# Performance work log

Measured on AMD Instinct MI355X. Metric: run time of the kernel, lower is better.

## Reference

```python
import jax, jax.numpy as jnp
import numpy as np
from jax import lax

EPS = 1e-12


def _l2norm(v):
    return v / (jnp.sqrt(jnp.sum(v * v)) + EPS)


def _spectral_norm(W, u):
    # one torch-style power iteration; u, v are treated as constants
    v = lax.stop_gradient(_l2norm(W.T @ u))
    u2 = lax.stop_gradient(_l2norm(W @ v))
    sigma = u2 @ (W @ v)
    return W / sigma


def _lstm(gates_x, Whh):
    # gates_x: [B, T, 4H] = x @ Wih^T + b_ih + b_hh, precomputed
    B, T, G = gates_x.shape
    H = G // 4
    WhhT = Whh.T  # [H, 4H]

    def step(carry, gx_t):
        h, c = carry
        gates = gx_t + h @ WhhT  # [B, 4H]
        i = jax.nn.sigmoid(gates[:, 0 * H:1 * H])
        f = jax.nn.sigmoid(gates[:, 1 * H:2 * H])
        g = jnp.tanh(gates[:, 2 * H:3 * H])
        o = jax.nn.sigmoid(gates[:, 3 * H:4 * H])
        c = f * c + i * g
        h = o * jnp.tanh(c)
        return (h, c), h

    h0 = jnp.zeros((B, H), gates_x.dtype)
    c0 = jnp.zeros((B, H), gates_x.dtype)
    _, hs = lax.scan(step, (h0, c0), jnp.swapaxes(gates_x, 0, 1))
    return jnp.swapaxes(hs, 0, 1)  # [B, T, H]


def setup_inputs() -> dict:
    key = jax.random.key(0)
    ks = jax.random.split(key, 8)
    B, T, C, H = 512, 512, 32, 128
    Cin = C + 1  # minibatch-std channel
    init = lambda k, shp: 0.02 * jax.random.normal(k, shp, dtype=jnp.float32)
    return {
        "x": jax.random.normal(ks[0], (B, T, C), dtype=jnp.float32),
        "w_ih_orig": init(ks[1], (4 * H, Cin)),
        "u_ih": _l2norm(jax.random.normal(ks[2], (4 * H,), dtype=jnp.float32)),
        "w_hh_orig": init(ks[3], (4 * H, H)),
        "u_hh": _l2norm(jax.random.normal(ks[4], (4 * H,), dtype=jnp.float32)),
        "b_ih": jnp.zeros((4 * H,), jnp.float32),
        "b_hh": jnp.zeros((4 * H,), jnp.float32),
        "attn_w": init(ks[5], (1, H)),
        "attn_b": jnp.zeros((1,), jnp.float32),
        "fc_w_orig": init(ks[6], (1, H)),
        "u_fc": _l2norm(jax.random.normal(ks[7], (1,), dtype=jnp.float32)),
        "fc_b": jnp.zeros((1,), jnp.float32),
    }


def reference(x, w_ih_orig, u_ih, w_hh_orig, u_hh, b_ih, b_hh,
              attn_w, attn_b, fc_w_orig, u_fc, fc_b):
    B = x.shape[0]
    # minibatch std feature (torch std: unbiased, ddof=1)
    std_per_step = jnp.std(x, axis=0, ddof=1, keepdims=True)        # [1,T,C]
    std_scalar = jnp.mean(std_per_step, axis=-1, keepdims=True)     # [1,T,1]
    std_channel = jnp.broadcast_to(std_scalar, (B,) + std_scalar.shape[1:])
    x = jnp.concatenate([x, std_channel], axis=-1)                  # [B,T,C+1]

    Wih = _spectral_norm(w_ih_orig, u_ih)
    Whh = _spectral_norm(w_hh_orig, u_hh)
    gates_x = jnp.einsum("btc,gc->btg", x, Wih) + b_ih + b_hh       # [B,T,4H]
    h = _lstm(gates_x, Whh)                                          # [B,T,H]

    attn_logits = jnp.einsum("bth,oh->bto", h, attn_w) + attn_b     # [B,T,1]
    attn = jax.nn.softmax(attn_logits, axis=1)
    pooled = jnp.sum(attn * h, axis=1)                               # [B,H]

    Wfc = _spectral_norm(fc_w_orig, u_fc)
    score = pooled @ Wfc.T + fc_b                                    # [B,1]
    return score
```

## Files before the change

### kernel.cpp

```cpp
#include <hip/hip_runtime.h>
#include <math.h>

#define TT 512
#define BB 512
#define CC 32
#define CIN 33
#define HH 128
#define EPSF 1e-12f
#define CH 16
#define NCH (TT / CH)
#define RB 2
#define HSP 160
#define GXP 520

typedef _Float16 half8 __attribute__((ext_vector_type(8)));
typedef _Float16 half2v __attribute__((ext_vector_type(2)));
typedef float f32x4 __attribute__((ext_vector_type(4)));

#define MFMA16H(a, b, c) __builtin_amdgcn_mfma_f32_16x16x32_f16(a, b, c, 0, 0, 0)
#define BARRIER() asm volatile("s_waitcnt lgkmcnt(0)\n\ts_barrier" ::: "memory")

__device__ __forceinline__ float fsig(float x) {
    return __builtin_amdgcn_rcpf(1.f + __expf(-x));
}
__device__ __forceinline__ float ftanh(float x) {
    return 1.f - 2.f * __builtin_amdgcn_rcpf(1.f + __expf(2.f * x));
}
__device__ __forceinline__ float wave_sum_dpp(float x) {
    x += __int_as_float(__builtin_amdgcn_update_dpp(0, __float_as_int(x), 0x111, 0xf, 0xf, true));
    x += __int_as_float(__builtin_amdgcn_update_dpp(0, __float_as_int(x), 0x112, 0xf, 0xf, true));
    x += __int_as_float(__builtin_amdgcn_update_dpp(0, __float_as_int(x), 0x114, 0xf, 0xf, true));
    x += __int_as_float(__builtin_amdgcn_update_dpp(0, __float_as_int(x), 0x118, 0xf, 0xf, true));
    x += __int_as_float(__builtin_amdgcn_update_dpp(0, __float_as_int(x), 0x142, 0xa, 0xf, true));
    x += __int_as_float(__builtin_amdgcn_update_dpp(0, __float_as_int(x), 0x143, 0xc, 0xf, true));
    return x;
}
__device__ __forceinline__ float row_sum_dpp(float x) {
    x += __int_as_float(__builtin_amdgcn_update_dpp(0, __float_as_int(x), 0x111, 0xf, 0xf, true));
    x += __int_as_float(__builtin_amdgcn_update_dpp(0, __float_as_int(x), 0x112, 0xf, 0xf, true));
    x += __int_as_float(__builtin_amdgcn_update_dpp(0, __float_as_int(x), 0x114, 0xf, 0xf, true));
    x += __int_as_float(__builtin_amdgcn_update_dpp(0, __float_as_int(x), 0x118, 0xf, 0xf, true));
    return x;
}
__device__ __forceinline__ float load_s(const float* p) {
    float v = __hip_atomic_load(p, __ATOMIC_RELAXED, __HIP_MEMORY_SCOPE_AGENT);
    for (int it = 0; it < 100000000 && __float_as_uint(v) == 0xAAAAAAAAu; ++it)
        v = __hip_atomic_load(p, __ATOMIC_RELAXED, __HIP_MEMORY_SCOPE_AGENT);
    return v;
}

__global__ __attribute__((amdgpu_flat_work_group_size(512, 512), amdgpu_waves_per_eu(2, 2)))
void critic_fused(
    const float* __restrict__ x,
    const float* __restrict__ w_ih, const float* __restrict__ u_ih,
    const float* __restrict__ w_hh, const float* __restrict__ u_hh,
    const float* __restrict__ b_ih, const float* __restrict__ b_hh,
    const float* __restrict__ attn_w, const float* __restrict__ attn_b,
    const float* __restrict__ fc_w, const float* __restrict__ u_fc,
    const float* __restrict__ fc_b,
    float* __restrict__ ws,
    float* __restrict__ out)
{
    const int tid = threadIdx.x;
    const int w   = tid >> 6;
    const int l   = tid & 63;
    const int m   = l & 15;
    const int q   = l >> 4;
    const int r   = q & 1;
    const int b0  = blockIdx.x * RB;
    const int jcol = 16 * w + m;

    __shared__ float4 sSS[2][8][8];
    __shared__ float4 sQQ[2][8][8];
    __shared__ float stdp[2][8];
    __shared__ float red[512];
    __shared__ float vv[128];
    __shared__ float sigS[3];
    __shared__ __align__(16) _Float16 hs[2][RB][HSP];
    __shared__ float gxs[2][2 * CH][GXP];
    __shared__ __align__(8) float bcast[2][RB];
    __shared__ float Sf[RB];
    __shared__ float part[8][RB];

    const int c4 = tid & 7;
    const int bs = tid >> 3;
    float4 xa[2][8];
#pragma unroll
    for (int tt = 0; tt < 2; ++tt) {
        const int t = 2 * blockIdx.x + tt;
#pragma unroll
        for (int i = 0; i < 8; ++i)
            xa[tt][i] = *reinterpret_cast<const float4*>(
                x + ((size_t)(bs * 8 + i) * TT + t) * CC + c4 * 4);
    }

    {
        const int c = tid & 127, qq = tid >> 7;
        const float* wp = w_hh + (size_t)(qq * 128) * HH + c;
        const float* up = u_hh + qq * 128;
        float a0 = 0.f, a1 = 0.f, a2 = 0.f, a3 = 0.f;
#pragma unroll 4
        for (int g = 0; g < 128; g += 4) {
            a0 = fmaf(wp[(size_t)(g + 0) * HH], up[g + 0], a0);
            a1 = fmaf(wp[(size_t)(g + 1) * HH], up[g + 1], a1);
            a2 = fmaf(wp[(size_t)(g + 2) * HH], up[g + 2], a2);
            a3 = fmaf(wp[(size_t)(g + 3) * HH], up[g + 3], a3);
        }
        red[tid] = (a0 + a1) + (a2 + a3);
    }

#pragma unroll
    for (int tt = 0; tt < 2; ++tt) {
        float4 S = make_float4(0.f, 0.f, 0.f, 0.f);
        float4 Q = make_float4(0.f, 0.f, 0.f, 0.f);
#pragma unroll
        for (int i = 0; i < 8; ++i) {
            float4 v = xa[tt][i];
            S.x += v.x; S.y += v.y; S.z += v.z; S.w += v.w;
            Q.x = fmaf(v.x, v.x, Q.x); Q.y = fmaf(v.y, v.y, Q.y);
            Q.z = fmaf(v.z, v.z, Q.z); Q.w = fmaf(v.w, v.w, Q.w);
        }
#pragma unroll
        for (int off = 8; off <= 32; off <<= 1) {
            S.x += __shfl_xor(S.x, off, 64); S.y += __shfl_xor(S.y, off, 64);
            S.z += __shfl_xor(S.z, off, 64); S.w += __shfl_xor(S.w, off, 64);
            Q.x += __shfl_xor(Q.x, off, 64); Q.y += __shfl_xor(Q.y, off, 64);
            Q.z += __shfl_xor(Q.z, off, 64); Q.w += __shfl_xor(Q.w, off, 64);
        }
        if (l < 8) { sSS[tt][w][c4] = S; sQQ[tt][w][c4] = Q; }
    }
    __syncthreads();

    if (tid < 128) vv[tid] = red[tid] + red[tid + 128] + red[tid + 256] + red[tid + 384];
    if (tid >= 384 && tid < 400) {
        const int tt2 = (tid - 384) >> 3, cc = (tid - 384) & 7;
        float4 St = make_float4(0.f, 0.f, 0.f, 0.f);
        float4 Qt = make_float4(0.f, 0.f, 0.f, 0.f);
#pragma unroll
        for (int i = 0; i < 8; ++i) {
            float4 a = sSS[tt2][i][cc], b4 = sQQ[tt2][i][cc];
            St.x += a.x; St.y += a.y; St.z += a.z; St.w += a.w;
            Qt.x += b4.x; Qt.y += b4.y; Qt.z += b4.z; Qt.w += b4.w;
        }
        float st = 0.f;
#pragma unroll
        for (int i = 0; i < 4; ++i) {
            float s1 = (i == 0) ? St.x : (i == 1) ? St.y : (i == 2) ? St.z : St.w;
            float q1 = (i == 0) ? Qt.x : (i == 1) ? Qt.y : (i == 2) ? Qt.z : Qt.w;
            float mean = s1 / 512.0f;
            float var  = (q1 - 512.0f * mean * mean) / 511.0f;
            st += sqrtf(fmaxf(var, 0.f));
        }
        stdp[tt2][cc] = st;
    }
    __syncthreads();
    if (tid >= 408 && tid < 410) {
        const int tt2 = tid - 408;
        float mm = 0.f;
#pragma unroll
        for (int i = 0; i < 8; ++i) mm += stdp[tt2][i];
        __hip_atomic_store(&ws[2 * blockIdx.x + tt2], mm / 32.0f, __ATOMIC_RELAXED,
                           __HIP_MEMORY_SCOPE_AGENT);
    }
    red[tid] = (tid < 128) ? vv[tid] * vv[tid] : 0.f;
    __syncthreads();

    {
        for (int s = 64; s >= 1; s >>= 1) { if (tid < s) red[tid] += red[tid + s]; __syncthreads(); }
        const float nv = sqrtf(red[0]);
        __syncthreads();
        if (tid < 128) vv[tid] = vv[tid] / (nv + EPSF);
        __syncthreads();
        float sq = 0.f;
        float2 vl = *reinterpret_cast<const float2*>(&vv[2 * l]);
#pragma unroll 4
        for (int gi = 0; gi < 64; ++gi) {
            const int g = w * 64 + gi;
            float2 wl = *reinterpret_cast<const float2*>(&w_hh[(size_t)g * HH + 2 * l]);
            float p  = fmaf(wl.x, vl.x, wl.y * vl.y);
            float tot = wave_sum_dpp(p);
            sq = fmaf(tot, tot, sq);
        }
        if (l == 63) red[w] = sq;
        __syncthreads();
        if (tid == 0) {
            float ns2 = 0.f;
            for (int i = 0; i < 8; ++i) ns2 += red[i];
            sigS[1] = ns2 / (sqrtf(ns2) + EPSF);
        }
        __syncthreads();
    }
    {
        if (l < CIN) {
            float a0 = 0.f, a1 = 0.f;
#pragma unroll 4
            for (int gi = 0; gi < 64; gi += 2) {
                const int g = w * 64 + gi;
                a0 = fmaf(w_ih[(size_t)(g + 0) * CIN + l], u_ih[g + 0], a0);
                a1 = fmaf(w_ih[(size_t)(g + 1) * CIN + l], u_ih[g + 1], a1);
            }
            red[w * 64 + l] = a0 + a1;
        }
        __syncthreads();
        if (tid < CIN) {
            float v = 0.f;
#pragma unroll
            for (int i = 0; i < 8; ++i) v += red[i * 64 + tid];
            vv[tid] = v;
        }
        __syncthreads();
        if (tid == 0) {
            float n2 = 0.f;
            for (int i = 0; i < CIN; ++i) n2 += vv[i] * vv[i];
            red[400] = sqrtf(n2);
        }
        __syncthreads();
        const float nv = red[400];
        if (tid < CIN) vv[tid] = vv[tid] / (nv + EPSF);
        __syncthreads();
        float vl = (l < CIN) ? vv[l] : 0.f;
        float sq = 0.f;
#pragma unroll 4
        for (int gi = 0; gi < 64; ++gi) {
            const int g = w * 64 + gi;
            float p = (l < CIN) ? w_ih[(size_t)g * CIN + l] * vl : 0.f;
            float tot = wave_sum_dpp(p);
            sq = fmaf(tot, tot, sq);
        }
        if (l == 63) red[w] = sq;
        __syncthreads();
        if (tid == 0) {
            float ns2 = 0.f;
            for (int i = 0; i < 8; ++i) ns2 += red[i];
            sigS[0] = ns2 / (sqrtf(ns2) + EPSF);
        }
        __syncthreads();
    }
    {
        red[tid] = (tid < 128) ? fc_w[tid] * fc_w[tid] : 0.f;
        __syncthreads();
        for (int s = 64; s >= 1; s >>= 1) { if (tid < s) red[tid] += red[tid + s]; __syncthreads(); }
        if (tid == 0) {
            float nw2 = red[0];
            float u0  = u_fc[0];
            float nv  = fabsf(u0) * sqrtf(nw2);
            float wv  = u0 * nw2 / (nv + EPSF);
            sigS[2]   = wv * wv / (fabsf(wv) + EPSF);
        }
        __syncthreads();
    }
    const float rih = 1.f / sigS[0];
    const float rhh = 1.f / sigS[1];
    const float rfc = 1.f / sigS[2];
    const float attb = attn_b[0];

    half8 Bf[4][5];
    float biasg[4], w32g[4];
#pragma unroll
    for (int p = 0; p < 4; ++p) {
        const int g = 16 * w + 128 * p + m;
#pragma unroll
        for (int kt = 0; kt < 4; ++kt) {
            const float* src = w_hh + (size_t)g * HH + kt * 32 + q * 8;
#pragma unroll
            for (int i = 0; i < 8; ++i) Bf[p][kt][i] = (_Float16)(src[i] * rhh);
        }
        {
            const float* src = w_ih + (size_t)g * CIN + q * 8;
#pragma unroll
            for (int i = 0; i < 8; ++i) Bf[p][4][i] = (_Float16)(src[i] * rih);
        }
        w32g[p]  = w_ih[(size_t)g * CIN + 32] * rih;
        biasg[p] = b_ih[g] + b_hh[g];
    }
    f32x4 zero4 = (f32x4){0.f, 0.f, 0.f, 0.f};
#pragma unroll
    for (int p = 0; p < 4; ++p) {
#pragma unroll
        for (int kt = 0; kt < 5; ++kt) asm volatile("" : "+v"(Bf[p][kt]));
        asm volatile("" : "+v"(biasg[p]), "+v"(w32g[p]));
    }
    asm volatile("" : "+v"(zero4));
    const float fcwj = fc_w[jcol] * rfc;
    const float aw0 = attn_w[2 * l];
    const float aw1 = attn_w[2 * l + 1];

#define STAGE_LOAD(t0_, xr_)                                                   \
    {                                                                          \
        _Pragma("unroll")                                                      \
        for (int mt = 0; mt < 2; ++mt) {                                       \
            const size_t base =                                                \
                ((size_t)(b0 + (m & 1)) * TT + ((t0_) + 8 * mt + (m >> 1))) *  \
                    CC + q * 8;                                                \
            xr_[mt][0] = *reinterpret_cast<const float4*>(x + base);           \
            xr_[mt][1] = *reinterpret_cast<const float4*>(x + base + 4);       \
        }                                                                      \
    }

#define STAGE_COMMIT(t0_, nb_, xr_)                                            \
    {                                                                          \
        _Pragma("unroll")                                                      \
        for (int mt = 0; mt < 2; ++mt) {                                       \
            half8 af = {(_Float16)xr_[mt][0].x, (_Float16)xr_[mt][0].y,        \
                        (_Float16)xr_[mt][0].z, (_Float16)xr_[mt][0].w,        \
                        (_Float16)xr_[mt][1].x, (_Float16)xr_[mt][1].y,        \
                        (_Float16)xr_[mt][1].z, (_Float16)xr_[mt][1].w};       \
            f32x4 s0 = MFMA16H(af, Bf[0][4], zero4);                           \
            f32x4 s1 = MFMA16H(af, Bf[1][4], zero4);                           \
            f32x4 s2 = MFMA16H(af, Bf[2][4], zero4);                           \
            f32x4 s3 = MFMA16H(af, Bf[3][4], zero4);                           \
            const float svl = load_s(&ws[(t0_) + 8 * mt + 2 * q]);             \
            const float svh = load_s(&ws[(t0_) + 8 * mt + 2 * q + 1]);         \
            const int row0 = 16 * mt + 4 * q;                                  \
            _Pragma("unroll")                                                  \
            for (int j = 0; j < 4; ++j) {                                      \
                const float sv = (j & 2) ? svh : svl;                          \
                gxs[nb_][row0 + j][jcol + 0]   = s0[j] + fmaf(w32g[0], sv, biasg[0]); \
                gxs[nb_][row0 + j][jcol + 128] = s1[j] + fmaf(w32g[1], sv, biasg[1]); \
                gxs[nb_][row0 + j][jcol + 256] = s2[j] + fmaf(w32g[2], sv, biasg[2]); \
                gxs[nb_][row0 + j][jcol + 384] = s3[j] + fmaf(w32g[3], sv, biasg[3]); \
            }                                                                  \
        }                                                                      \
    }

#define LSTM_STEP(t_, k_, cb_)                                                 \
    {                                                                          \
        const int t  = (t_);                                                   \
        const int hb = (t + 1) & 1;                                            \
        half8 ah0 = *(const half8*)&hs[hb][m & 1][0 * 32 + q * 8];             \
        half8 ah1 = *(const half8*)&hs[hb][m & 1][1 * 32 + q * 8];             \
        half8 ah2 = *(const half8*)&hs[hb][m & 1][2 * 32 + q * 8];             \
        half8 ah3 = *(const half8*)&hs[hb][m & 1][3 * 32 + q * 8];             \
        const float* gxr = &gxs[cb_][((k_) << 1) | r][jcol];                   \
        float gx0 = gxr[0];                                                    \
        float gx1 = gxr[128];                                                  \
        float gx2 = gxr[256];                                                  \
        float gx3 = gxr[384];                                                  \
        float dotp = 0.f;                                                      \
        if (t > 0 && w >= 6) {                                                 \
            half2v hh = *(const half2v*)&hs[hb][w - 6][2 * l];                 \
            dotp = fmaf(aw0, (float)hh[0], aw1 * (float)hh[1]);                \
        }                                                                      \
        if (t >= 2) P = fmaf(bcast[(t - 1) & 1][r], hpp, P);                   \
        f32x4 acc0 = MFMA16H(ah0, Bf[0][0], zero4);                            \
        f32x4 acc1 = MFMA16H(ah0, Bf[1][0], zero4);                            \
        f32x4 acc2 = MFMA16H(ah0, Bf[2][0], zero4);                            \
        f32x4 acc3 = MFMA16H(ah0, Bf[3][0], zero4);                            \
        acc0 = MFMA16H(ah1, Bf[0][1], acc0);                                   \
        acc1 = MFMA16H(ah1, Bf[1][1], acc1);                                   \
        acc2 = MFMA16H(ah1, Bf[2][1], acc2);                                   \
        acc3 = MFMA16H(ah1, Bf[3][1], acc3);                                   \
        acc0 = MFMA16H(ah2, Bf[0][2], acc0);                                   \
        acc1 = MFMA16H(ah2, Bf[1][2], acc1);                                   \
        acc2 = MFMA16H(ah2, Bf[2][2], acc2);                                   \
        acc3 = MFMA16H(ah2, Bf[3][2], acc3);                                   \
        acc0 = MFMA16H(ah3, Bf[0][3], acc0);                                   \
        acc1 = MFMA16H(ah3, Bf[1][3], acc1);                                   \
        acc2 = MFMA16H(ah3, Bf[2][3], acc2);                                   \
        acc3 = MFMA16H(ah3, Bf[3][3], acc3);                                   \
        if (t > 0 && w >= 6) {                                                 \
            float tot = wave_sum_dpp(dotp);                                    \
            if (l == 63) {                                                     \
                float beta = __expf(tot + attb);                               \
                Sreg += beta;                                                  \
                bcast[t & 1][w - 6] = beta;                                    \
            }                                                                  \
        }                                                                      \
        {                                                                      \
            float g0 = acc0[r] + gx0;                                          \
            float g1 = acc1[r] + gx1;                                          \
            float g2 = acc2[r] + gx2;                                          \
            float g3 = acc3[r] + gx3;                                          \
            float ig = fsig(g0);                                               \
            float fg = fsig(g1);                                               \
            float gg = ftanh(g2);                                              \
            float og = fsig(g3);                                               \
            c_st = fmaf(fg, c_st, ig * gg);                                    \
            float hv = og * ftanh(c_st);                                       \
            hpp   = hprev;                                                     \
            hprev = hv;                                                        \
            if (q < 2) hs[t & 1][r][jcol] = (_Float16)hv;                      \
        }                                                                      \
        BARRIER();                                                             \
    }

    for (int i = tid; i < 2 * RB * HSP; i += 512) (&hs[0][0][0])[i] = (_Float16)0.f;

    float c_st = 0.f, P = 0.f, hprev = 0.f, hpp = 0.f;
    float Sreg = 0.f;

    {
        float4 xr0[2][2];
        STAGE_LOAD(0, xr0);
        STAGE_COMMIT(0, 0, xr0);
    }
    __syncthreads();

    for (int tc = 0; tc < NCH; ++tc) {
        const int cb  = tc & 1;
        const int t0n = (tc + 1) * CH;
        float4 xr[2][2];
        if (tc + 1 < NCH) STAGE_LOAD(t0n, xr);
#pragma unroll 2
        for (int k = 0; k < CH / 2; ++k) LSTM_STEP(tc * CH + k, k, cb);
        if (tc + 1 < NCH) STAGE_COMMIT(t0n, cb ^ 1, xr);
#pragma unroll 2
        for (int k = CH / 2; k < CH; ++k) LSTM_STEP(tc * CH + k, k, cb);
    }

    P = fmaf(bcast[1][r], hpp, P);
    if (w >= 6) {
        half2v hh = *(const half2v*)&hs[1][w - 6][2 * l];
        float dotp = fmaf(aw0, (float)hh[0], aw1 * (float)hh[1]);
        float tot = wave_sum_dpp(dotp);
        if (l == 63) {
            float beta = __expf(tot + attb);
            Sreg += beta;
            bcast[0][w - 6] = beta;
            Sf[w - 6] = Sreg;
        }
    }
    __syncthreads();
    {
        float Pv = fmaf(bcast[0][r], hprev, P);
        float v  = Pv * __builtin_amdgcn_rcpf(Sf[r]) * fcwj;
        float rs = row_sum_dpp(v);
        if (l == 15) part[w][0] = rs;
        if (l == 31) part[w][1] = rs;
    }
    __syncthreads();
    if (tid < RB) {
        float a = 0.f;
#pragma unroll
        for (int i = 0; i < 8; ++i) a += part[i][tid];
        out[b0 + tid] = a + fc_b[0];
    }
}

extern "C" void kernel_launch(void* const* d_in, const int* in_sizes, int n_in,
                              void* d_out, int out_size, void* d_ws, size_t ws_size,
                              hipStream_t stream) {
    const float* x      = (const float*)d_in[0];
    const float* w_ih   = (const float*)d_in[1];
    const float* u_ih   = (const float*)d_in[2];
    const float* w_hh   = (const float*)d_in[3];
    const float* u_hh   = (const float*)d_in[4];
    const float* b_ih   = (const float*)d_in[5];
    const float* b_hh   = (const float*)d_in[6];
    const float* attn_w = (const float*)d_in[7];
    const float* attn_b = (const float*)d_in[8];
    const float* fc_w   = (const float*)d_in[9];
    const float* u_fc   = (const float*)d_in[10];
    const float* fc_b   = (const float*)d_in[11];
    float* ws  = (float*)d_ws;
    float* out = (float*)d_out;

    critic_fused<<<BB / RB, 512, 0, stream>>>(x, w_ih, u_ih, w_hh, u_hh, b_ih, b_hh,
                                              attn_w, attn_b, fc_w, u_fc, fc_b, ws, out);
}
```

Before: 471.7 us.

## Process one batch row per block with 512 blocks and interleaved gate layout

Each workgroup now handles one batch element instead of two, so the launch uses 512 blocks and the wave occupancy hint rises from 2 to 4 waves per EU. The precomputed input-gate buffer is laid out interleaved per column, so each step reads all four gate values with a single vector load. This roughly halves shared memory per block, which allows more blocks resident at once to cover the latency of the serial LSTM recurrence. The trade-off is that each step's MFMA tile uses only one useful row, so half the matrix work of the two-row version is wasted, and the 4-waves hint may limit registers. The per-timestep std values are still published through the workspace and polled by consumers.

```diff
diff --git a/kernel.cpp b/kernel.cpp
--- a/kernel.cpp
+++ b/kernel.cpp
@@ -9,9 +9,8 @@
 #define EPSF 1e-12f
 #define CH 16
 #define NCH (TT / CH)
-#define RB 2
 #define HSP 160
-#define GXP 520
+#define GXSTR 516
 
 typedef _Float16 half8 __attribute__((ext_vector_type(8)));
 typedef _Float16 half2v __attribute__((ext_vector_type(2)));
@@ -49,7 +48,7 @@
     return v;
 }
 
-__global__ __attribute__((amdgpu_flat_work_group_size(512, 512), amdgpu_waves_per_eu(2, 2)))
+__global__ __attribute__((amdgpu_flat_work_group_size(512, 512), amdgpu_waves_per_eu(4, 4)))
 void critic_fused(
     const float* __restrict__ x,
     const float* __restrict__ w_ih, const float* __restrict__ u_ih,
@@ -66,33 +65,28 @@
     const int l   = tid & 63;
     const int m   = l & 15;
     const int q   = l >> 4;
-    const int r   = q & 1;
-    const int b0  = blockIdx.x * RB;
+    const int b0  = blockIdx.x;
     const int jcol = 16 * w + m;
 
-    __shared__ float4 sSS[2][8][8];
-    __shared__ float4 sQQ[2][8][8];
-    __shared__ float stdp[2][8];
+    __shared__ float4 sSS[8][8];
+    __shared__ float4 sQQ[8][8];
+    __shared__ float stdp[8];
     __shared__ float red[512];
     __shared__ float vv[128];
     __shared__ float sigS[3];
-    __shared__ __align__(16) _Float16 hs[2][RB][HSP];
-    __shared__ float gxs[2][2 * CH][GXP];
-    __shared__ __align__(8) float bcast[2][RB];
-    __shared__ float Sf[RB];
-    __shared__ float part[8][RB];
+    __shared__ __align__(16) _Float16 hs[2][HSP];
+    __shared__ __align__(16) float gxs[2][CH][GXSTR];
+    __shared__ float bcast[2];
+    __shared__ float SfS;
+    __shared__ float part[8];
 
     const int c4 = tid & 7;
     const int bs = tid >> 3;
-    float4 xa[2][8];
-#pragma unroll
-    for (int tt = 0; tt < 2; ++tt) {
-        const int t = 2 * blockIdx.x + tt;
-#pragma unroll
-        for (int i = 0; i < 8; ++i)
-            xa[tt][i] = *reinterpret_cast<const float4*>(
-                x + ((size_t)(bs * 8 + i) * TT + t) * CC + c4 * 4);
-    }
+    float4 xa[8];
+#pragma unroll
+    for (int i = 0; i < 8; ++i)
+        xa[i] = *reinterpret_cast<const float4*>(
+            x + ((size_t)(bs * 8 + i) * TT + b0) * CC + c4 * 4);
 
     {
         const int c = tid & 127, qq = tid >> 7;
@@ -109,13 +103,12 @@
         red[tid] = (a0 + a1) + (a2 + a3);
     }
 
-#pragma unroll
-    for (int tt = 0; tt < 2; ++tt) {
+    {
         float4 S = make_float4(0.f, 0.f, 0.f, 0.f);
         float4 Q = make_float4(0.f, 0.f, 0.f, 0.f);
 #pragma unroll
         for (int i = 0; i < 8; ++i) {
-            float4 v = xa[tt][i];
+            float4 v = xa[i];
             S.x += v.x; S.y += v.y; S.z += v.z; S.w += v.w;
             Q.x = fmaf(v.x, v.x, Q.x); Q.y = fmaf(v.y, v.y, Q.y);
             Q.z = fmaf(v.z, v.z, Q.z); Q.w = fmaf(v.w, v.w, Q.w);
@@ -127,18 +120,18 @@
             Q.x += __shfl_xor(Q.x, off, 64); Q.y += __shfl_xor(Q.y, off, 64);
             Q.z += __shfl_xor(Q.z, off, 64); Q.w += __shfl_xor(Q.w, off, 64);
         }
-        if (l < 8) { sSS[tt][w][c4] = S; sQQ[tt][w][c4] = Q; }
+        if (l < 8) { sSS[w][c4] = S; sQQ[w][c4] = Q; }
     }
     __syncthreads();
 
     if (tid < 128) vv[tid] = red[tid] + red[tid + 128] + red[tid + 256] + red[tid + 384];
-    if (tid >= 384 && tid < 400) {
-        const int tt2 = (tid - 384) >> 3, cc = (tid - 384) & 7;
+    if (tid >= 384 && tid < 392) {
+        const int cc = tid - 384;
         float4 St = make_float4(0.f, 0.f, 0.f, 0.f);
         float4 Qt = make_float4(0.f, 0.f, 0.f, 0.f);
 #pragma unroll
         for (int i = 0; i < 8; ++i) {
-            float4 a = sSS[tt2][i][cc], b4 = sQQ[tt2][i][cc];
+            float4 a = sSS[i][cc], b4 = sQQ[i][cc];
             St.x += a.x; St.y += a.y; St.z += a.z; St.w += a.w;
             Qt.x += b4.x; Qt.y += b4.y; Qt.z += b4.z; Qt.w += b4.w;
         }
@@ -151,15 +144,14 @@
             float var  = (q1 - 512.0f * mean * mean) / 511.0f;
             st += sqrtf(fmaxf(var, 0.f));
         }
-        stdp[tt2][cc] = st;
-    }
-    __syncthreads();
-    if (tid >= 408 && tid < 410) {
-        const int tt2 = tid - 408;
+        stdp[cc] = st;
+    }
+    __syncthreads();
+    if (tid == 408) {
         float mm = 0.f;
 #pragma unroll
-        for (int i = 0; i < 8; ++i) mm += stdp[tt2][i];
-        __hip_atomic_store(&ws[2 * blockIdx.x + tt2], mm / 32.0f, __ATOMIC_RELAXED,
+        for (int i = 0; i < 8; ++i) mm += stdp[i];
+        __hip_atomic_store(&ws[b0], mm / 32.0f, __ATOMIC_RELAXED,
                            __HIP_MEMORY_SCOPE_AGENT);
     }
     red[tid] = (tid < 128) ? vv[tid] * vv[tid] : 0.f;
@@ -287,39 +279,35 @@
 
 #define STAGE_LOAD(t0_, xr_)                                                   \
     {                                                                          \
-        _Pragma("unroll")                                                      \
-        for (int mt = 0; mt < 2; ++mt) {                                       \
-            const size_t base =                                                \
-                ((size_t)(b0 + (m & 1)) * TT + ((t0_) + 8 * mt + (m >> 1))) *  \
-                    CC + q * 8;                                                \
-            xr_[mt][0] = *reinterpret_cast<const float4*>(x + base);           \
-            xr_[mt][1] = *reinterpret_cast<const float4*>(x + base + 4);       \
-        }                                                                      \
+        const size_t base = ((size_t)b0 * TT + (t0_) + m) * CC + q * 8;        \
+        xr_[0] = *reinterpret_cast<const float4*>(x + base);                   \
+        xr_[1] = *reinterpret_cast<const float4*>(x + base + 4);               \
     }
 
 #define STAGE_COMMIT(t0_, nb_, xr_)                                            \
     {                                                                          \
+        half8 af = {(_Float16)xr_[0].x, (_Float16)xr_[0].y,                    \
+                    (_Float16)xr_[0].z, (_Float16)xr_[0].w,                    \
+                    (_Float16)xr_[1].x, (_Float16)xr_[1].y,                    \
+                    (_Float16)xr_[1].z, (_Float16)xr_[1].w};                   \
+        f32x4 s0 = MFMA16H(af, Bf[0][4], zero4);                               \
+        f32x4 s1 = MFMA16H(af, Bf[1][4], zero4);                               \
+        f32x4 s2 = MFMA16H(af, Bf[2][4], zero4);                               \
+        f32x4 s3 = MFMA16H(af, Bf[3][4], zero4);                               \
+        const int row0 = 4 * q;                                                \
+        const float sv0 = load_s(&ws[(t0_) + row0 + 0]);                       \
+        const float sv1 = load_s(&ws[(t0_) + row0 + 1]);                       \
+        const float sv2 = load_s(&ws[(t0_) + row0 + 2]);                       \
+        const float sv3 = load_s(&ws[(t0_) + row0 + 3]);                       \
         _Pragma("unroll")                                                      \
-        for (int mt = 0; mt < 2; ++mt) {                                       \
-            half8 af = {(_Float16)xr_[mt][0].x, (_Float16)xr_[mt][0].y,        \
-                        (_Float16)xr_[mt][0].z, (_Float16)xr_[mt][0].w,        \
-                        (_Float16)xr_[mt][1].x, (_Float16)xr_[mt][1].y,        \
-                        (_Float16)xr_[mt][1].z, (_Float16)xr_[mt][1].w};       \
-            f32x4 s0 = MFMA16H(af, Bf[0][4], zero4);                           \
-            f32x4 s1 = MFMA16H(af, Bf[1][4], zero4);                           \
-            f32x4 s2 = MFMA16H(af, Bf[2][4], zero4);                           \
-            f32x4 s3 = MFMA16H(af, Bf[3][4], zero4);                           \
-            const float svl = load_s(&ws[(t0_) + 8 * mt + 2 * q]);             \
-            const float svh = load_s(&ws[(t0_) + 8 * mt + 2 * q + 1]);         \
-            const int row0 = 16 * mt + 4 * q;                                  \
-            _Pragma("unroll")                                                  \
-            for (int j = 0; j < 4; ++j) {                                      \
-                const float sv = (j & 2) ? svh : svl;                          \
-                gxs[nb_][row0 + j][jcol + 0]   = s0[j] + fmaf(w32g[0], sv, biasg[0]); \
-                gxs[nb_][row0 + j][jcol + 128] = s1[j] + fmaf(w32g[1], sv, biasg[1]); \
-                gxs[nb_][row0 + j][jcol + 256] = s2[j] + fmaf(w32g[2], sv, biasg[2]); \
-                gxs[nb_][row0 + j][jcol + 384] = s3[j] + fmaf(w32g[3], sv, biasg[3]); \
-            }                                                                  \
+        for (int j = 0; j < 4; ++j) {                                          \
+            const float sv = (j == 0) ? sv0 : (j == 1) ? sv1 : (j == 2) ? sv2 : sv3; \
+            f32x4 gv;                                                          \
+            gv[0] = s0[j] + fmaf(w32g[0], sv, biasg[0]);                       \
+            gv[1] = s1[j] + fmaf(w32g[1], sv, biasg[1]);                       \
+            gv[2] = s2[j] + fmaf(w32g[2], sv, biasg[2]);                       \
+            gv[3] = s3[j] + fmaf(w32g[3], sv, biasg[3]);                       \
+            *reinterpret_cast<f32x4*>(&gxs[nb_][row0 + j][jcol * 4]) = gv;     \
         }                                                                      \
     }
 
@@ -327,21 +315,17 @@
     {                                                                          \
         const int t  = (t_);                                                   \
         const int hb = (t + 1) & 1;                                            \
-        half8 ah0 = *(const half8*)&hs[hb][m & 1][0 * 32 + q * 8];             \
-        half8 ah1 = *(const half8*)&hs[hb][m & 1][1 * 32 + q * 8];             \
-        half8 ah2 = *(const half8*)&hs[hb][m & 1][2 * 32 + q * 8];             \
-        half8 ah3 = *(const half8*)&hs[hb][m & 1][3 * 32 + q * 8];             \
-        const float* gxr = &gxs[cb_][((k_) << 1) | r][jcol];                   \
-        float gx0 = gxr[0];                                                    \
-        float gx1 = gxr[128];                                                  \
-        float gx2 = gxr[256];                                                  \
-        float gx3 = gxr[384];                                                  \
+        half8 ah0 = *(const half8*)&hs[hb][0 * 32 + q * 8];                    \
+        half8 ah1 = *(const half8*)&hs[hb][1 * 32 + q * 8];                    \
+        half8 ah2 = *(const half8*)&hs[hb][2 * 32 + q * 8];                    \
+        half8 ah3 = *(const half8*)&hs[hb][3 * 32 + q * 8];                    \
+        f32x4 gx4 = *reinterpret_cast<const f32x4*>(&gxs[cb_][k_][jcol * 4]);  \
         float dotp = 0.f;                                                      \
-        if (t > 0 && w >= 6) {                                                 \
-            half2v hh = *(const half2v*)&hs[hb][w - 6][2 * l];                 \
+        if (t > 0 && w == 7) {                                                 \
+            half2v hh = *(const half2v*)&hs[hb][2 * l];                        \
             dotp = fmaf(aw0, (float)hh[0], aw1 * (float)hh[1]);                \
         }                                                                      \
-        if (t >= 2) P = fmaf(bcast[(t - 1) & 1][r], hpp, P);                   \
+        if (t >= 2) P = fmaf(bcast[(t - 1) & 1], hpp, P);                      \
         f32x4 acc0 = MFMA16H(ah0, Bf[0][0], zero4);                            \
         f32x4 acc1 = MFMA16H(ah0, Bf[1][0], zero4);                            \
         f32x4 acc2 = MFMA16H(ah0, Bf[2][0], zero4);                            \
@@ -358,19 +342,19 @@
         acc1 = MFMA16H(ah3, Bf[1][3], acc1);                                   \
         acc2 = MFMA16H(ah3, Bf[2][3], acc2);                                   \
         acc3 = MFMA16H(ah3, Bf[3][3], acc3);                                   \
-        if (t > 0 && w >= 6) {                                                 \
+        if (t > 0 && w == 7) {                                                 \
             float tot = wave_sum_dpp(dotp);                                    \
             if (l == 63) {                                                     \
                 float beta = __expf(tot + attb);                               \
                 Sreg += beta;                                                  \
-                bcast[t & 1][w - 6] = beta;                                    \
+                bcast[t & 1] = beta;                                           \
             }                                                                  \
         }                                                                      \
         {                                                                      \
-            float g0 = acc0[r] + gx0;                                          \
-            float g1 = acc1[r] + gx1;                                          \
-            float g2 = acc2[r] + gx2;                                          \
-            float g3 = acc3[r] + gx3;                                          \
+            float g0 = acc0[0] + gx4[0];                                       \
+            float g1 = acc1[0] + gx4[1];                                       \
+            float g2 = acc2[0] + gx4[2];                                       \
+            float g3 = acc3[0] + gx4[3];                                       \
             float ig = fsig(g0);                                               \
             float fg = fsig(g1);                                               \
             float gg = ftanh(g2);                                              \
@@ -379,18 +363,18 @@
             float hv = og * ftanh(c_st);                                       \
             hpp   = hprev;                                                     \
             hprev = hv;                                                        \
-            if (q < 2) hs[t & 1][r][jcol] = (_Float16)hv;                      \
+            if (q == 0) hs[t & 1][jcol] = (_Float16)hv;                        \
         }                                                                      \
         BARRIER();                                                             \
     }
 
-    for (int i = tid; i < 2 * RB * HSP; i += 512) (&hs[0][0][0])[i] = (_Float16)0.f;
+    for (int i = tid; i < 2 * HSP; i += 512) (&hs[0][0])[i] = (_Float16)0.f;
 
     float c_st = 0.f, P = 0.f, hprev = 0.f, hpp = 0.f;
     float Sreg = 0.f;
 
     {
-        float4 xr0[2][2];
+        float4 xr0[2];
         STAGE_LOAD(0, xr0);
         STAGE_COMMIT(0, 0, xr0);
     }
@@ -399,7 +383,7 @@
     for (int tc = 0; tc < NCH; ++tc) {
         const int cb  = tc & 1;
         const int t0n = (tc + 1) * CH;
-        float4 xr[2][2];
+        float4 xr[2];
         if (tc + 1 < NCH) STAGE_LOAD(t0n, xr);
 #pragma unroll 2
         for (int k = 0; k < CH / 2; ++k) LSTM_STEP(tc * CH + k, k, cb);
@@ -408,32 +392,31 @@
         for (int k = CH / 2; k < CH; ++k) LSTM_STEP(tc * CH + k, k, cb);
     }
 
-    P = fmaf(bcast[1][r], hpp, P);
-    if (w >= 6) {
-        half2v hh = *(const half2v*)&hs[1][w - 6][2 * l];
+    P = fmaf(bcast[1], hpp, P);
+    if (w == 7) {
+        half2v hh = *(const half2v*)&hs[1][2 * l];
         float dotp = fmaf(aw0, (float)hh[0], aw1 * (float)hh[1]);
         float tot = wave_sum_dpp(dotp);
         if (l == 63) {
             float beta = __expf(tot + attb);
             Sreg += beta;
-            bcast[0][w - 6] = beta;
-            Sf[w - 6] = Sreg;
-        }
-    }
-    __syncthreads();
-    {
-        float Pv = fmaf(bcast[0][r], hprev, P);
-        float v  = Pv * __builtin_amdgcn_rcpf(Sf[r]) * fcwj;
+            bcast[0] = beta;
+            SfS = Sreg;
+        }
+    }
+    __syncthreads();
+    {
+        float Pv = fmaf(bcast[0], hprev, P);
+        float v  = Pv * __builtin_amdgcn_rcpf(SfS) * fcwj;
         float rs = row_sum_dpp(v);
-        if (l == 15) part[w][0] = rs;
-        if (l == 31) part[w][1] = rs;
-    }
-    __syncthreads();
-    if (tid < RB) {
+        if (l == 15) part[w] = rs;
+    }
+    __syncthreads();
+    if (tid == 0) {
         float a = 0.f;
 #pragma unroll
-        for (int i = 0; i < 8; ++i) a += part[i][tid];
-        out[b0 + tid] = a + fc_b[0];
+        for (int i = 0; i < 8; ++i) a += part[i];
+        out[b0] = a + fc_b[0];
     }
 }
 
@@ -455,6 +438,6 @@
     float* ws  = (float*)d_ws;
     float* out = (float*)d_out;
 
-    critic_fused<<<BB / RB, 512, 0, stream>>>(x, w_ih, u_ih, w_hh, u_hh, b_ih, b_hh,
-                                              attn_w, attn_b, fc_w, u_fc, fc_b, ws, out);
-}
+    critic_fused<<<BB, 512, 0, stream>>>(x, w_ih, u_ih, w_hh, u_hh, b_ih, b_hh,
+                                         attn_w, attn_b, fc_w, u_fc, fc_b, ws, out);
+}
```

Result: slower. 630.7 us (+33.7%).

## Interleave gate-x buffer by batch row and split recurrent MFMAs per row

Applied to the files above, without the earlier changes.

Reorganizes the precomputed input-gate buffer so the four gate values for one column and batch row sit contiguously, letting each step read them with one 16-byte LDS load instead of four scalar loads. The recurrent matmul now broadcasts each batch row's hidden state across all 16 MFMA rows and issues two separate MFMA chains, one per batch row, taking element 0 of each. This doubles the MFMA count per step but removes the per-lane gather by r. The attention logit work moves from waves 6-7 to waves 0-1.

```diff
diff --git a/kernel.cpp b/kernel.cpp
--- a/kernel.cpp
+++ b/kernel.cpp
@@ -77,7 +77,7 @@
     __shared__ float vv[128];
     __shared__ float sigS[3];
     __shared__ __align__(16) _Float16 hs[2][RB][HSP];
-    __shared__ float gxs[2][2 * CH][GXP];
+    __shared__ __align__(16) float gxs[2][CH][RB][GXP];
     __shared__ __align__(8) float bcast[2][RB];
     __shared__ float Sf[RB];
     __shared__ float part[8][RB];
@@ -311,14 +311,16 @@
             f32x4 s3 = MFMA16H(af, Bf[3][4], zero4);                           \
             const float svl = load_s(&ws[(t0_) + 8 * mt + 2 * q]);             \
             const float svh = load_s(&ws[(t0_) + 8 * mt + 2 * q + 1]);         \
-            const int row0 = 16 * mt + 4 * q;                                  \
             _Pragma("unroll")                                                  \
             for (int j = 0; j < 4; ++j) {                                      \
                 const float sv = (j & 2) ? svh : svl;                          \
-                gxs[nb_][row0 + j][jcol + 0]   = s0[j] + fmaf(w32g[0], sv, biasg[0]); \
-                gxs[nb_][row0 + j][jcol + 128] = s1[j] + fmaf(w32g[1], sv, biasg[1]); \
-                gxs[nb_][row0 + j][jcol + 256] = s2[j] + fmaf(w32g[2], sv, biasg[2]); \
-                gxs[nb_][row0 + j][jcol + 384] = s3[j] + fmaf(w32g[3], sv, biasg[3]); \
+                f32x4 gv;                                                      \
+                gv[0] = s0[j] + fmaf(w32g[0], sv, biasg[0]);                   \
+                gv[1] = s1[j] + fmaf(w32g[1], sv, biasg[1]);                   \
+                gv[2] = s2[j] + fmaf(w32g[2], sv, biasg[2]);                   \
+                gv[3] = s3[j] + fmaf(w32g[3], sv, biasg[3]);                   \
+                *reinterpret_cast<f32x4*>(                                     \
+                    &gxs[nb_][8 * mt + 2 * q + (j >> 1)][j & 1][jcol * 4]) = gv; \
             }                                                                  \
         }                                                                      \
     }
@@ -327,50 +329,67 @@
     {                                                                          \
         const int t  = (t_);                                                   \
         const int hb = (t + 1) & 1;                                            \
-        half8 ah0 = *(const half8*)&hs[hb][m & 1][0 * 32 + q * 8];             \
-        half8 ah1 = *(const half8*)&hs[hb][m & 1][1 * 32 + q * 8];             \
-        half8 ah2 = *(const half8*)&hs[hb][m & 1][2 * 32 + q * 8];             \
-        half8 ah3 = *(const half8*)&hs[hb][m & 1][3 * 32 + q * 8];             \
-        const float* gxr = &gxs[cb_][((k_) << 1) | r][jcol];                   \
-        float gx0 = gxr[0];                                                    \
-        float gx1 = gxr[128];                                                  \
-        float gx2 = gxr[256];                                                  \
-        float gx3 = gxr[384];                                                  \
+        half8 a00 = *(const half8*)&hs[hb][0][0 * 32 + q * 8];                 \
+        half8 a01 = *(const half8*)&hs[hb][0][1 * 32 + q * 8];                 \
+        half8 a02 = *(const half8*)&hs[hb][0][2 * 32 + q * 8];                 \
+        half8 a03 = *(const half8*)&hs[hb][0][3 * 32 + q * 8];                 \
+        half8 a10 = *(const half8*)&hs[hb][1][0 * 32 + q * 8];                 \
+        half8 a11 = *(const half8*)&hs[hb][1][1 * 32 + q * 8];                 \
+        half8 a12 = *(const half8*)&hs[hb][1][2 * 32 + q * 8];                 \
+        half8 a13 = *(const half8*)&hs[hb][1][3 * 32 + q * 8];                 \
+        f32x4 gx4 = *reinterpret_cast<const f32x4*>(&gxs[cb_][k_][r][jcol * 4]); \
         float dotp = 0.f;                                                      \
-        if (t > 0 && w >= 6) {                                                 \
-            half2v hh = *(const half2v*)&hs[hb][w - 6][2 * l];                 \
+        if (t > 0 && w < RB) {                                                 \
+            half2v hh = *(const half2v*)&hs[hb][w][2 * l];                     \
             dotp = fmaf(aw0, (float)hh[0], aw1 * (float)hh[1]);                \
         }                                                                      \
         if (t >= 2) P = fmaf(bcast[(t - 1) & 1][r], hpp, P);                   \
-        f32x4 acc0 = MFMA16H(ah0, Bf[0][0], zero4);                            \
-        f32x4 acc1 = MFMA16H(ah0, Bf[1][0], zero4);                            \
-        f32x4 acc2 = MFMA16H(ah0, Bf[2][0], zero4);                            \
-        f32x4 acc3 = MFMA16H(ah0, Bf[3][0], zero4);                            \
-        acc0 = MFMA16H(ah1, Bf[0][1], acc0);                                   \
-        acc1 = MFMA16H(ah1, Bf[1][1], acc1);                                   \
-        acc2 = MFMA16H(ah1, Bf[2][1], acc2);                                   \
-        acc3 = MFMA16H(ah1, Bf[3][1], acc3);                                   \
-        acc0 = MFMA16H(ah2, Bf[0][2], acc0);                                   \
-        acc1 = MFMA16H(ah2, Bf[1][2], acc1);                                   \
-        acc2 = MFMA16H(ah2, Bf[2][2], acc2);                                   \
-        acc3 = MFMA16H(ah2, Bf[3][2], acc3);                                   \
-        acc0 = MFMA16H(ah3, Bf[0][3], acc0);                                   \
-        acc1 = MFMA16H(ah3, Bf[1][3], acc1);                                   \
-        acc2 = MFMA16H(ah3, Bf[2][3], acc2);                                   \
-        acc3 = MFMA16H(ah3, Bf[3][3], acc3);                                   \
-        if (t > 0 && w >= 6) {                                                 \
+        f32x4 acc0 = MFMA16H(a00, Bf[0][0], zero4);                            \
+        f32x4 acc1 = MFMA16H(a00, Bf[1][0], zero4);                            \
+        f32x4 acc2 = MFMA16H(a00, Bf[2][0], zero4);                            \
+        f32x4 acc3 = MFMA16H(a00, Bf[3][0], zero4);                            \
+        acc0 = MFMA16H(a01, Bf[0][1], acc0);                                   \
+        acc1 = MFMA16H(a01, Bf[1][1], acc1);                                   \
+        acc2 = MFMA16H(a01, Bf[2][1], acc2);                                   \
+        acc3 = MFMA16H(a01, Bf[3][1], acc3);                                   \
+        acc0 = MFMA16H(a02, Bf[0][2], acc0);                                   \
+        acc1 = MFMA16H(a02, Bf[1][2], acc1);                                   \
+        acc2 = MFMA16H(a02, Bf[2][2], acc2);                                   \
+        acc3 = MFMA16H(a02, Bf[3][2], acc3);                                   \
+        acc0 = MFMA16H(a03, Bf[0][3], acc0);                                   \
+        acc1 = MFMA16H(a03, Bf[1][3], acc1);                                   \
+        acc2 = MFMA16H(a03, Bf[2][3], acc2);                                   \
+        acc3 = MFMA16H(a03, Bf[3][3], acc3);                                   \
+        const float g00 = acc0[0], g01 = acc1[0], g02 = acc2[0], g03 = acc3[0];\
+        f32x4 bcc0 = MFMA16H(a10, Bf[0][0], zero4);                            \
+        f32x4 bcc1 = MFMA16H(a10, Bf[1][0], zero4);                            \
+        f32x4 bcc2 = MFMA16H(a10, Bf[2][0], zero4);                            \
+        f32x4 bcc3 = MFMA16H(a10, Bf[3][0], zero4);                            \
+        bcc0 = MFMA16H(a11, Bf[0][1], bcc0);                                   \
+        bcc1 = MFMA16H(a11, Bf[1][1], bcc1);                                   \
+        bcc2 = MFMA16H(a11, Bf[2][1], bcc2);                                   \
+        bcc3 = MFMA16H(a11, Bf[3][1], bcc3);                                   \
+        bcc0 = MFMA16H(a12, Bf[0][2], bcc0);                                   \
+        bcc1 = MFMA16H(a12, Bf[1][2], bcc1);                                   \
+        bcc2 = MFMA16H(a12, Bf[2][2], bcc2);                                   \
+        bcc3 = MFMA16H(a12, Bf[3][2], bcc3);                                   \
+        bcc0 = MFMA16H(a13, Bf[0][3], bcc0);                                   \
+        bcc1 = MFMA16H(a13, Bf[1][3], bcc1);                                   \
+        bcc2 = MFMA16H(a13, Bf[2][3], bcc2);                                   \
+        bcc3 = MFMA16H(a13, Bf[3][3], bcc3);                                   \
+        if (t > 0 && w < RB) {                                                 \
             float tot = wave_sum_dpp(dotp);                                    \
             if (l == 63) {                                                     \
                 float beta = __expf(tot + attb);                               \
                 Sreg += beta;                                                  \
-                bcast[t & 1][w - 6] = beta;                                    \
+                bcast[t & 1][w] = beta;                                        \
             }                                                                  \
         }                                                                      \
         {                                                                      \
-            float g0 = acc0[r] + gx0;                                          \
-            float g1 = acc1[r] + gx1;                                          \
-            float g2 = acc2[r] + gx2;                                          \
-            float g3 = acc3[r] + gx3;                                          \
+            float g0 = (r ? bcc0[0] : g00) + gx4[0];                           \
+            float g1 = (r ? bcc1[0] : g01) + gx4[1];                           \
+            float g2 = (r ? bcc2[0] : g02) + gx4[2];                           \
+            float g3 = (r ? bcc3[0] : g03) + gx4[3];                           \
             float ig = fsig(g0);                                               \
             float fg = fsig(g1);                                               \
             float gg = ftanh(g2);                                              \
@@ -409,15 +428,15 @@
     }
 
     P = fmaf(bcast[1][r], hpp, P);
-    if (w >= 6) {
-        half2v hh = *(const half2v*)&hs[1][w - 6][2 * l];
+    if (w < RB) {
+        half2v hh = *(const half2v*)&hs[1][w][2 * l];
         float dotp = fmaf(aw0, (float)hh[0], aw1 * (float)hh[1]);
         float tot = wave_sum_dpp(dotp);
         if (l == 63) {
             float beta = __expf(tot + attb);
             Sreg += beta;
-            bcast[0][w - 6] = beta;
-            Sf[w - 6] = Sreg;
+            bcast[0][w] = beta;
+            Sf[w] = Sreg;
         }
     }
     __syncthreads();
```

Result: slower. 553.1 us (+17.2%).

## Restructure LSTM loop: distribute attention logits, vectorize gate loads, reload Wih per commit

Applied to the files above, without the earlier changes.

Computes the attention logit inside each LSTM step using per-wave row sums written to a small partial buffer, so the separate wave-reduction path on waves 6-7 goes away. Gate-input staging is re-laid out as [t][b][h*4] so each lane reads its four gates with one 16-byte LDS load. The input-projection weights are no longer kept in registers; they are reloaded from global memory at each chunk commit, which frees VGPRs. The x prefetch, ws spin-loads and commit are spread across separate steps within the chunk. The trade-off is extra global loads per commit and an added DPP reduction on every step's critical path.

```diff
diff --git a/kernel.cpp b/kernel.cpp
--- a/kernel.cpp
+++ b/kernel.cpp
@@ -14,7 +14,6 @@
 #define GXP 520
 
 typedef _Float16 half8 __attribute__((ext_vector_type(8)));
-typedef _Float16 half2v __attribute__((ext_vector_type(2)));
 typedef float f32x4 __attribute__((ext_vector_type(4)));
 
 #define MFMA16H(a, b, c) __builtin_amdgcn_mfma_f32_16x16x32_f16(a, b, c, 0, 0, 0)
@@ -68,7 +67,7 @@
     const int q   = l >> 4;
     const int r   = q & 1;
     const int b0  = blockIdx.x * RB;
-    const int jcol = 16 * w + m;
+    const int hcol = 16 * w + m;
 
     __shared__ float4 sSS[2][8][8];
     __shared__ float4 sQQ[2][8][8];
@@ -77,10 +76,11 @@
     __shared__ float vv[128];
     __shared__ float sigS[3];
     __shared__ __align__(16) _Float16 hs[2][RB][HSP];
-    __shared__ float gxs[2][2 * CH][GXP];
-    __shared__ __align__(8) float bcast[2][RB];
+    __shared__ __align__(16) float gxs[2][CH][RB][GXP];
+    __shared__ __align__(16) float bcast[2][RB];
+    __shared__ float part[2][8][RB];
     __shared__ float Sf[RB];
-    __shared__ float part[8][RB];
+    __shared__ float fcp[8][RB];
 
     const int c4 = tid & 7;
     const int bs = tid >> 3;
@@ -253,75 +253,80 @@
     const float rhh = 1.f / sigS[1];
     const float rfc = 1.f / sigS[2];
     const float attb = attn_b[0];
-
-    half8 Bf[4][5];
-    float biasg[4], w32g[4];
-#pragma unroll
-    for (int p = 0; p < 4; ++p) {
-        const int g = 16 * w + 128 * p + m;
+    const float awj  = attn_w[hcol];
+    const float fcwj = fc_w[hcol] * rfc;
+
+    half8 BREG[4][4];
+#pragma unroll
+    for (int g = 0; g < 4; ++g) {
+        const int gcol = 128 * g + hcol;
 #pragma unroll
         for (int kt = 0; kt < 4; ++kt) {
-            const float* src = w_hh + (size_t)g * HH + kt * 32 + q * 8;
-#pragma unroll
-            for (int i = 0; i < 8; ++i) Bf[p][kt][i] = (_Float16)(src[i] * rhh);
-        }
-        {
-            const float* src = w_ih + (size_t)g * CIN + q * 8;
-#pragma unroll
-            for (int i = 0; i < 8; ++i) Bf[p][4][i] = (_Float16)(src[i] * rih);
-        }
-        w32g[p]  = w_ih[(size_t)g * CIN + 32] * rih;
-        biasg[p] = b_ih[g] + b_hh[g];
+            const float* src = w_hh + (size_t)gcol * HH + kt * 32 + q * 8;
+#pragma unroll
+            for (int i = 0; i < 8; ++i) BREG[g][kt][i] = (_Float16)(src[i] * rhh);
+        }
     }
     f32x4 zero4 = (f32x4){0.f, 0.f, 0.f, 0.f};
 #pragma unroll
-    for (int p = 0; p < 4; ++p) {
-#pragma unroll
-        for (int kt = 0; kt < 5; ++kt) asm volatile("" : "+v"(Bf[p][kt]));
-        asm volatile("" : "+v"(biasg[p]), "+v"(w32g[p]));
-    }
+    for (int g = 0; g < 4; ++g)
+#pragma unroll
+        for (int kt = 0; kt < 4; ++kt) asm volatile("" : "+v"(BREG[g][kt]));
     asm volatile("" : "+v"(zero4));
-    const float fcwj = fc_w[jcol] * rfc;
-    const float aw0 = attn_w[2 * l];
-    const float aw1 = attn_w[2 * l + 1];
-
-#define STAGE_LOAD(t0_, xr_)                                                   \
-    {                                                                          \
+
+#define XLOAD(t0_)                                                             \
+    do {                                                                       \
         _Pragma("unroll")                                                      \
         for (int mt = 0; mt < 2; ++mt) {                                       \
             const size_t base =                                                \
                 ((size_t)(b0 + (m & 1)) * TT + ((t0_) + 8 * mt + (m >> 1))) *  \
                     CC + q * 8;                                                \
-            xr_[mt][0] = *reinterpret_cast<const float4*>(x + base);           \
-            xr_[mt][1] = *reinterpret_cast<const float4*>(x + base + 4);       \
+            xr[mt][0] = *reinterpret_cast<const float4*>(x + base);            \
+            xr[mt][1] = *reinterpret_cast<const float4*>(x + base + 4);        \
         }                                                                      \
-    }
-
-#define STAGE_COMMIT(t0_, nb_, xr_)                                            \
-    {                                                                          \
+    } while (0)
+
+#define WSPIN(t0_)                                                             \
+    do {                                                                       \
+        svr[0] = load_s(&ws[(t0_) + 2 * q]);                                   \
+        svr[1] = load_s(&ws[(t0_) + 2 * q + 1]);                               \
+        svr[2] = load_s(&ws[(t0_) + 8 + 2 * q]);                               \
+        svr[3] = load_s(&ws[(t0_) + 8 + 2 * q + 1]);                           \
+    } while (0)
+
+#define COMMIT(nb_)                                                            \
+    do {                                                                       \
         _Pragma("unroll")                                                      \
         for (int mt = 0; mt < 2; ++mt) {                                       \
-            half8 af = {(_Float16)xr_[mt][0].x, (_Float16)xr_[mt][0].y,        \
-                        (_Float16)xr_[mt][0].z, (_Float16)xr_[mt][0].w,        \
-                        (_Float16)xr_[mt][1].x, (_Float16)xr_[mt][1].y,        \
-                        (_Float16)xr_[mt][1].z, (_Float16)xr_[mt][1].w};       \
-            f32x4 s0 = MFMA16H(af, Bf[0][4], zero4);                           \
-            f32x4 s1 = MFMA16H(af, Bf[1][4], zero4);                           \
-            f32x4 s2 = MFMA16H(af, Bf[2][4], zero4);                           \
-            f32x4 s3 = MFMA16H(af, Bf[3][4], zero4);                           \
-            const float svl = load_s(&ws[(t0_) + 8 * mt + 2 * q]);             \
-            const float svh = load_s(&ws[(t0_) + 8 * mt + 2 * q + 1]);         \
-            const int row0 = 16 * mt + 4 * q;                                  \
+            half8 af = {(_Float16)xr[mt][0].x, (_Float16)xr[mt][0].y,          \
+                        (_Float16)xr[mt][0].z, (_Float16)xr[mt][0].w,          \
+                        (_Float16)xr[mt][1].x, (_Float16)xr[mt][1].y,          \
+                        (_Float16)xr[mt][1].z, (_Float16)xr[mt][1].w};         \
+            f32x4 sg[4]; float w32g[4], biasg[4];                              \
+            _Pragma("unroll")                                                  \
+            for (int g = 0; g < 4; ++g) {                                      \
+                const int gcol = 128 * g + hcol;                               \
+                const float* wsrc = w_ih + (size_t)gcol * CIN;                 \
+                half8 wf;                                                      \
+                _Pragma("unroll")                                              \
+                for (int i = 0; i < 8; ++i) wf[i] = (_Float16)(wsrc[q * 8 + i] * rih); \
+                sg[g] = MFMA16H(af, wf, zero4);                                \
+                w32g[g]  = wsrc[32] * rih;                                     \
+                biasg[g] = b_ih[gcol] + b_hh[gcol];                            \
+            }                                                                  \
             _Pragma("unroll")                                                  \
             for (int j = 0; j < 4; ++j) {                                      \
-                const float sv = (j & 2) ? svh : svl;                          \
-                gxs[nb_][row0 + j][jcol + 0]   = s0[j] + fmaf(w32g[0], sv, biasg[0]); \
-                gxs[nb_][row0 + j][jcol + 128] = s1[j] + fmaf(w32g[1], sv, biasg[1]); \
-                gxs[nb_][row0 + j][jcol + 256] = s2[j] + fmaf(w32g[2], sv, biasg[2]); \
-                gxs[nb_][row0 + j][jcol + 384] = s3[j] + fmaf(w32g[3], sv, biasg[3]); \
+                const float sv = (j & 2) ? svr[2 * mt + 1] : svr[2 * mt];      \
+                f32x4 gv;                                                      \
+                gv[0] = sg[0][j] + fmaf(w32g[0], sv, biasg[0]);                \
+                gv[1] = sg[1][j] + fmaf(w32g[1], sv, biasg[1]);                \
+                gv[2] = sg[2][j] + fmaf(w32g[2], sv, biasg[2]);                \
+                gv[3] = sg[3][j] + fmaf(w32g[3], sv, biasg[3]);                \
+                *reinterpret_cast<f32x4*>(                                     \
+                    &gxs[nb_][8 * mt + 2 * q + (j >> 1)][j & 1][hcol * 4]) = gv; \
             }                                                                  \
         }                                                                      \
-    }
+    } while (0)
 
 #define LSTM_STEP(t_, k_, cb_)                                                 \
     {                                                                          \
@@ -331,46 +336,38 @@
         half8 ah1 = *(const half8*)&hs[hb][m & 1][1 * 32 + q * 8];             \
         half8 ah2 = *(const half8*)&hs[hb][m & 1][2 * 32 + q * 8];             \
         half8 ah3 = *(const half8*)&hs[hb][m & 1][3 * 32 + q * 8];             \
-        const float* gxr = &gxs[cb_][((k_) << 1) | r][jcol];                   \
-        float gx0 = gxr[0];                                                    \
-        float gx1 = gxr[128];                                                  \
-        float gx2 = gxr[256];                                                  \
-        float gx3 = gxr[384];                                                  \
-        float dotp = 0.f;                                                      \
-        if (t > 0 && w >= 6) {                                                 \
-            half2v hh = *(const half2v*)&hs[hb][w - 6][2 * l];                 \
-            dotp = fmaf(aw0, (float)hh[0], aw1 * (float)hh[1]);                \
+        f32x4 gx4 = *reinterpret_cast<const f32x4*>(&gxs[cb_][k_][r][hcol * 4]); \
+        if (t >= 2) P = fmaf(bcast[t & 1][r], hpp, P);                         \
+        if (w == 7 && l < 2 && t >= 1) {                                       \
+            const int pp = (t - 1) & 1;                                        \
+            float logit = attb;                                                \
+            _Pragma("unroll")                                                  \
+            for (int i = 0; i < 8; ++i) logit += part[pp][i][l];               \
+            float beta = __expf(logit);                                        \
+            Sreg += beta;                                                      \
+            bcast[pp][l] = beta;                                               \
         }                                                                      \
-        if (t >= 2) P = fmaf(bcast[(t - 1) & 1][r], hpp, P);                   \
-        f32x4 acc0 = MFMA16H(ah0, Bf[0][0], zero4);                            \
-        f32x4 acc1 = MFMA16H(ah0, Bf[1][0], zero4);                            \
-        f32x4 acc2 = MFMA16H(ah0, Bf[2][0], zero4);                            \
-        f32x4 acc3 = MFMA16H(ah0, Bf[3][0], zero4);                            \
-        acc0 = MFMA16H(ah1, Bf[0][1], acc0);                                   \
-        acc1 = MFMA16H(ah1, Bf[1][1], acc1);                                   \
-        acc2 = MFMA16H(ah1, Bf[2][1], acc2);                                   \
-        acc3 = MFMA16H(ah1, Bf[3][1], acc3);                                   \
-        acc0 = MFMA16H(ah2, Bf[0][2], acc0);                                   \
-        acc1 = MFMA16H(ah2, Bf[1][2], acc1);                                   \
-        acc2 = MFMA16H(ah2, Bf[2][2], acc2);                                   \
-        acc3 = MFMA16H(ah2, Bf[3][2], acc3);                                   \
-        acc0 = MFMA16H(ah3, Bf[0][3], acc0);                                   \
-        acc1 = MFMA16H(ah3, Bf[1][3], acc1);                                   \
-        acc2 = MFMA16H(ah3, Bf[2][3], acc2);                                   \
-        acc3 = MFMA16H(ah3, Bf[3][3], acc3);                                   \
-        if (t > 0 && w >= 6) {                                                 \
-            float tot = wave_sum_dpp(dotp);                                    \
-            if (l == 63) {                                                     \
-                float beta = __expf(tot + attb);                               \
-                Sreg += beta;                                                  \
-                bcast[t & 1][w - 6] = beta;                                    \
-            }                                                                  \
-        }                                                                      \
+        f32x4 A0 = MFMA16H(ah0, BREG[0][0], zero4);                            \
+        f32x4 A1 = MFMA16H(ah0, BREG[1][0], zero4);                            \
+        f32x4 A2 = MFMA16H(ah0, BREG[2][0], zero4);                            \
+        f32x4 A3 = MFMA16H(ah0, BREG[3][0], zero4);                            \
+        A0 = MFMA16H(ah1, BREG[0][1], A0);                                     \
+        A1 = MFMA16H(ah1, BREG[1][1], A1);                                     \
+        A2 = MFMA16H(ah1, BREG[2][1], A2);                                     \
+        A3 = MFMA16H(ah1, BREG[3][1], A3);                                     \
+        A0 = MFMA16H(ah2, BREG[0][2], A0);                                     \
+        A1 = MFMA16H(ah2, BREG[1][2], A1);                                     \
+        A2 = MFMA16H(ah2, BREG[2][2], A2);                                     \
+        A3 = MFMA16H(ah2, BREG[3][2], A3);                                     \
+        A0 = MFMA16H(ah3, BREG[0][3], A0);                                     \
+        A1 = MFMA16H(ah3, BREG[1][3], A1);                                     \
+        A2 = MFMA16H(ah3, BREG[2][3], A2);                                     \
+        A3 = MFMA16H(ah3, BREG[3][3], A3);                                     \
         {                                                                      \
-            float g0 = acc0[r] + gx0;                                          \
-            float g1 = acc1[r] + gx1;                                          \
-            float g2 = acc2[r] + gx2;                                          \
-            float g3 = acc3[r] + gx3;                                          \
+            float g0 = (r ? A0[1] : A0[0]) + gx4[0];                           \
+            float g1 = (r ? A1[1] : A1[0]) + gx4[1];                           \
+            float g2 = (r ? A2[1] : A2[0]) + gx4[2];                           \
+            float g3 = (r ? A3[1] : A3[0]) + gx4[3];                           \
             float ig = fsig(g0);                                               \
             float fg = fsig(g1);                                               \
             float gg = ftanh(g2);                                              \
@@ -379,7 +376,10 @@
             float hv = og * ftanh(c_st);                                       \
             hpp   = hprev;                                                     \
             hprev = hv;                                                        \
-            if (q < 2) hs[t & 1][r][jcol] = (_Float16)hv;                      \
+            if (q < 2) hs[t & 1][q][hcol] = (_Float16)hv;                      \
+            float pr = (q < 2) ? awj * hv : 0.f;                               \
+            float rs = row_sum_dpp(pr);                                        \
+            if ((l & 15) == 15 && q < 2) part[t & 1][w][q] = rs;               \
         }                                                                      \
         BARRIER();                                                             \
     }
@@ -388,51 +388,53 @@
 
     float c_st = 0.f, P = 0.f, hprev = 0.f, hpp = 0.f;
     float Sreg = 0.f;
-
-    {
-        float4 xr0[2][2];
-        STAGE_LOAD(0, xr0);
-        STAGE_COMMIT(0, 0, xr0);
+    float4 xr[2][2];
+    float svr[4];
+
+    {
+        XLOAD(0);
+        WSPIN(0);
+        COMMIT(0);
     }
     __syncthreads();
 
     for (int tc = 0; tc < NCH; ++tc) {
         const int cb  = tc & 1;
         const int t0n = (tc + 1) * CH;
-        float4 xr[2][2];
-        if (tc + 1 < NCH) STAGE_LOAD(t0n, xr);
 #pragma unroll 2
-        for (int k = 0; k < CH / 2; ++k) LSTM_STEP(tc * CH + k, k, cb);
-        if (tc + 1 < NCH) STAGE_COMMIT(t0n, cb ^ 1, xr);
-#pragma unroll 2
-        for (int k = CH / 2; k < CH; ++k) LSTM_STEP(tc * CH + k, k, cb);
-    }
-
-    P = fmaf(bcast[1][r], hpp, P);
-    if (w >= 6) {
-        half2v hh = *(const half2v*)&hs[1][w - 6][2 * l];
-        float dotp = fmaf(aw0, (float)hh[0], aw1 * (float)hh[1]);
-        float tot = wave_sum_dpp(dotp);
-        if (l == 63) {
-            float beta = __expf(tot + attb);
-            Sreg += beta;
-            bcast[0][w - 6] = beta;
-            Sf[w - 6] = Sreg;
-        }
-    }
-    __syncthreads();
-    {
-        float Pv = fmaf(bcast[0][r], hprev, P);
-        float v  = Pv * __builtin_amdgcn_rcpf(Sf[r]) * fcwj;
-        float rs = row_sum_dpp(v);
-        if (l == 15) part[w][0] = rs;
-        if (l == 31) part[w][1] = rs;
+        for (int k = 0; k < CH; ++k) {
+            LSTM_STEP(tc * CH + k, k, cb);
+            if (tc + 1 < NCH) {
+                if (k == 0) XLOAD(t0n);
+                else if (k == 2) WSPIN(t0n);
+                else if (k == 8) COMMIT(cb ^ 1);
+            }
+        }
+    }
+
+    P = fmaf(bcast[0][r], hpp, P);
+    if (w == 7 && l < 2) {
+        float logit = attb;
+#pragma unroll
+        for (int i = 0; i < 8; ++i) logit += part[1][i][l];
+        float beta = __expf(logit);
+        Sreg += beta;
+        bcast[1][l] = beta;
+        Sf[l] = Sreg;
+    }
+    __syncthreads();
+    P = fmaf(bcast[1][r], hprev, P);
+    {
+        float Pv = P * __builtin_amdgcn_rcpf(Sf[r]) * fcwj;
+        float pr = (q < 2) ? Pv : 0.f;
+        float rs = row_sum_dpp(pr);
+        if ((l & 15) == 15 && q < 2) fcp[w][q] = rs;
     }
     __syncthreads();
     if (tid < RB) {
         float a = 0.f;
 #pragma unroll
-        for (int i = 0; i < 8; ++i) a += part[i][tid];
+        for (int i = 0; i < 8; ++i) a += fcp[i][tid];
         out[b0 + tid] = a + fc_b[0];
     }
 }
```

After: 518.8 us. +10.0%, slower.
